# Performance work log

Hardware: AMD Instinct MI355X
Metric: run time of the kernel (lower is better)

The kernel has to match this reference:

```python
import jax, jax.numpy as jnp
import numpy as np

CONF_THRES = 0.1
IOU_THRES = 0.6
MAX_DET = 300
MAX_WH = 4096.0  # class offset for non-agnostic NMS
NEG_SLOPE = 0.01  # nn.LeakyReLU default


def xywh2xyxy(p):
    xy, wh = p[..., :2], p[..., 2:4]
    return jnp.concatenate([xy - wh / 2, xy + wh / 2], axis=-1)


def pairwise_iou(a, b):
    area_a = (a[:, 2] - a[:, 0]) * (a[:, 3] - a[:, 1])
    area_b = (b[:, 2] - b[:, 0]) * (b[:, 3] - b[:, 1])
    lt = jnp.maximum(a[:, None, :2], b[None, :, :2])
    rb = jnp.minimum(a[:, None, 2:], b[None, :, 2:])
    wh = jnp.clip(rb - lt, 0.0)
    inter = wh[..., 0] * wh[..., 1]
    return inter / (area_a[:, None] + area_b[None, :] - inter + 1e-7)


def nms_single(pred):  # pred: [N, 5+nc]
    boxes = xywh2xyxy(pred[:, :4])
    scores = pred[:, 5:] * pred[:, 4:5]  # obj * cls
    conf = jnp.max(scores, axis=1)
    cls = jnp.argmax(scores, axis=1)
    conf = jnp.where(conf > CONF_THRES, conf, 0.0)
    topv, topi = jax.lax.top_k(conf, MAX_DET)
    b = boxes[topi]                      # [K,4]
    c = cls[topi]
    valid = topv > CONF_THRES
    bo = b + (c.astype(b.dtype) * MAX_WH)[:, None]  # class-offset boxes
    iou = pairwise_iou(bo, bo)           # [K,K]
    idx = jnp.arange(MAX_DET)
    def body(i, keep):
        sup = keep[i] & (iou[i] > IOU_THRES) & (idx > i)
        return keep & ~sup
    keep = jax.lax.fori_loop(0, MAX_DET, body, valid)
    return b, keep


def bilinear_sample(feat, y, x):  # feat [C,H,W], y/x [K,P] -> [C,K,P]
    C, H, W = feat.shape
    y = jnp.clip(y, 0.0, H - 1.0)
    x = jnp.clip(x, 0.0, W - 1.0)
    y0 = jnp.floor(y).astype(jnp.int32)
    x0 = jnp.floor(x).astype(jnp.int32)
    y1 = jnp.minimum(y0 + 1, H - 1)
    x1 = jnp.minimum(x0 + 1, W - 1)
    ly = y - y0
    lx = x - x0
    return (feat[:, y0, x0] * ((1 - ly) * (1 - lx))
            + feat[:, y0, x1] * ((1 - ly) * lx)
            + feat[:, y1, x0] * (ly * (1 - lx))
            + feat[:, y1, x1] * (ly * lx))


def roi_align_1x1(feat, boxes, scale):  # feat [C,H,W], boxes [K,4] xyxy (input-px)
    b = boxes * scale
    w = jnp.maximum(b[:, 2] - b[:, 0], 1.0)
    h = jnp.maximum(b[:, 3] - b[:, 1], 1.0)
    off = jnp.array([0.5, 1.5], dtype=boxes.dtype)
    xs = b[:, 0:1] + off[None, :] * (w[:, None] / 2.0)  # [K,2]
    ys = b[:, 1:2] + off[None, :] * (h[:, None] / 2.0)
    yy = ys[:, jnp.array([0, 0, 1, 1])]  # [K,4] 2x2 grid
    xx = xs[:, jnp.array([0, 1, 0, 1])]
    v = bilinear_sample(feat, yy, xx)    # [C,K,4]
    return jnp.mean(v, axis=2).T         # [K,C]


def rescale_boxes(bbox, hw, hw0):  # scale_coords + normalize by orig shape
    gain = jnp.minimum(hw[0] / hw0[0], hw[1] / hw0[1])
    pad_x = (hw[1] - hw0[1] * gain) / 2.0
    pad_y = (hw[0] - hw0[0] * gain) / 2.0
    x1 = jnp.clip((bbox[:, 0] - pad_x) / gain, 0.0, hw0[1])
    y1 = jnp.clip((bbox[:, 1] - pad_y) / gain, 0.0, hw0[0])
    x2 = jnp.clip((bbox[:, 2] - pad_x) / gain, 0.0, hw0[1])
    y2 = jnp.clip((bbox[:, 3] - pad_y) / gain, 0.0, hw0[0])
    # divide by shapes[i][0] indexed [w,h,w,h]
    return jnp.stack([x1 / hw0[1], y1 / hw0[0], x2 / hw0[1], y2 / hw0[0]], axis=1)


def setup_inputs() -> dict:
    key = jax.random.key(0)
    ks = jax.random.split(key, 10)
    B, N, NC = 8, 25500, 80
    xy = jax.random.uniform(ks[0], (B, N, 2), minval=0.0, maxval=640.0)
    wh = jax.random.uniform(ks[1], (B, N, 2), minval=8.0, maxval=160.0)
    obj = jax.random.uniform(ks[2], (B, N, 1))
    cls = jax.random.uniform(ks[3], (B, N, NC))
    preds = jnp.concatenate([xy, wh, obj, cls], axis=-1)
    feat1 = jax.random.normal(ks[4], (B, 128, 80, 80), dtype=jnp.float32)
    feat2 = jax.random.normal(ks[5], (B, 256, 40, 40), dtype=jnp.float32)
    feat3 = jax.random.normal(ks[6], (B, 512, 20, 20), dtype=jnp.float32)
    feat4 = jax.random.normal(ks[7], (B, 1024, 10, 10), dtype=jnp.float32)
    orig_hw = jnp.tile(jnp.array([[720.0, 1280.0]], dtype=jnp.float32), (B, 1))
    W1 = jax.random.normal(ks[8], (1920, 256), dtype=jnp.float32) * 0.02
    b1 = jnp.zeros((256,), dtype=jnp.float32)
    W2 = jax.random.normal(ks[9], (256, 256), dtype=jnp.float32) * 0.02
    b2 = jnp.zeros((256,), dtype=jnp.float32)
    return {"preds": preds, "feat1": feat1, "feat2": feat2, "feat3": feat3,
            "feat4": feat4, "orig_hw": orig_hw, "W1": W1, "b1": b1,
            "W2": W2, "b2": b2}


def reference(preds, feat1, feat2, feat3, feat4, orig_hw, W1, b1, W2, b2):
    preds = jax.lax.stop_gradient(preds)  # out.detach() in the original
    hw = jnp.array(feat1.shape[-2:], dtype=preds.dtype) * 8.0  # network input h,w
    boxes, keep = jax.vmap(nms_single)(preds)  # [B,K,4], [B,K]
    f1 = jax.vmap(lambda f, b: roi_align_1x1(f, b, 1.0 / 8))(feat1, boxes)
    f2 = jax.vmap(lambda f, b: roi_align_1x1(f, b, 1.0 / 16))(feat2, boxes)
    f3 = jax.vmap(lambda f, b: roi_align_1x1(f, b, 1.0 / 32))(feat3, boxes)
    f4 = jax.vmap(lambda f, b: roi_align_1x1(f, b, 1.0 / 64))(feat4, boxes)
    f = jnp.concatenate([f1, f2, f3, f4], axis=-1)  # [B,K,1920]
    h = jax.nn.leaky_relu(f @ W1 + b1, NEG_SLOPE)
    h = jax.nn.leaky_relu(h @ W2 + b2, NEG_SLOPE)   # [B,K,256]
    bb = jax.vmap(lambda b, s: rescale_boxes(b, hw, s))(boxes, orig_hw)
    out = jnp.concatenate([bb, h], axis=-1)  # [B,K,260]
    return out * keep[..., None].astype(out.dtype)
```

## Files before the change

kernel.cpp:

```cpp
#include <hip/hip_runtime.h>
#include <hip/hip_bf16.h>
#include <cstdint>
#include <cstddef>

#define NBATCH 8
#define NANCH 25500
#define MAXDET 300
#define NBINS 2048
#define CAP 2048

typedef __bf16 bf16x8 __attribute__((ext_vector_type(8)));
typedef float floatx4 __attribute__((ext_vector_type(4)));
typedef unsigned long long ull;

__device__ __forceinline__ int conf_bin(float v) {
  unsigned bits = __float_as_uint(v);
  int bin = (int)((bits - 0x3D800000u) >> 14);
  return bin > (NBINS - 1) ? (NBINS - 1) : bin;
}

#define CONF_TILE 64
__global__ __launch_bounds__(256) void conf_kernel(const float* __restrict__ preds,
                                                   float* __restrict__ conf,
                                                   int* __restrict__ cls,
                                                   int* __restrict__ ghist, int total) {
  if (blockIdx.x < 16) {
    #pragma unroll
    for (int k = 0; k < 4; ++k)
      ghist[blockIdx.x * 1024 + k * 256 + threadIdx.x] = 0;
  }
  __shared__ float s[CONF_TILE * 85];
  int base = blockIdx.x * CONF_TILE;
  int nA = total - base; if (nA > CONF_TILE) nA = CONF_TILE;
  int n4 = (nA * 85) >> 2;
  const float4* g4 = (const float4*)(preds + (size_t)base * 85);
  float4* s4 = (float4*)s;
  for (int i = threadIdx.x; i < n4; i += 256) s4[i] = g4[i];
  __syncthreads();
  int lane16 = threadIdx.x & 15;
  int sub = threadIdx.x >> 4;
  #pragma unroll
  for (int r = 0; r < 4; ++r) {
    int a = r * 16 + sub;
    if (a < nA) {
      const float* row = s + a * 85;
      float obj = row[4];
      float best = -1.0f; int bc = 0;
      #pragma unroll
      for (int j = 0; j < 5; ++j) {
        int c = lane16 * 5 + j;
        float v = row[5 + c] * obj;
        if (v > best) { best = v; bc = c; }
      }
      #pragma unroll
      for (int m = 1; m < 16; m <<= 1) {
        float ov = __shfl_xor(best, m, 64);
        int   oc = __shfl_xor(bc,   m, 64);
        if (ov > best || (ov == best && oc < bc)) { best = ov; bc = oc; }
      }
      if (lane16 == 0) {
        int idx = base + a;
        conf[idx] = (best > 0.1f) ? best : 0.0f;
        cls[idx] = bc;
      }
    }
  }
}

struct TransArgs {
  const float* src[6];
  __hip_bfloat16* dst[6];
  int C[6], HW[6], tx[6], tpb[6], start[6];
};

__global__ void transpose_all_kernel(TransArgs a, const float* __restrict__ conf,
                                     int* __restrict__ ghist) {
  __shared__ __align__(16) char msm[8192];
  int bid = blockIdx.x;
  if (bid < 64) {
    int* sh = (int*)msm;
    int b = bid >> 3, seg = bid & 7;
    int tid = threadIdx.y * 32 + threadIdx.x;
    for (int i = tid; i < NBINS; i += 256) sh[i] = 0;
    __syncthreads();
    const int N4 = NANCH >> 2;
    int i0 = (N4 * seg) >> 3, i1 = (N4 * (seg + 1)) >> 3;
    const float4* cf4 = (const float4*)(conf + (size_t)b * NANCH);
    for (int i = i0 + tid; i < i1; i += 256) {
      float4 v = cf4[i];
      if (v.x > 0.1f) atomicAdd(&sh[conf_bin(v.x)], 1);
      if (v.y > 0.1f) atomicAdd(&sh[conf_bin(v.y)], 1);
      if (v.z > 0.1f) atomicAdd(&sh[conf_bin(v.z)], 1);
      if (v.w > 0.1f) atomicAdd(&sh[conf_bin(v.w)], 1);
    }
    __syncthreads();
    for (int i = tid; i < NBINS; i += 256) {
      int c = sh[i];
      if (c) atomicAdd(&ghist[b * NBINS + i], c);
    }
    return;
  }
  int bid2 = bid - 64;
  float (*tile)[33] = (float(*)[33])msm;
  int s = 0;
  #pragma unroll
  for (int i = 1; i < 6; ++i) if (bid2 >= a.start[i]) s = i;
  int local = bid2 - a.start[s];
  int C = a.C[s], HW = a.HW[s], tx0 = a.tx[s], tpb = a.tpb[s];
  int b = local / tpb;
  int rem = local - b * tpb;
  int p0 = (rem % tx0) * 32;
  int c0 = (rem / tx0) * 32;
  const float* inb = a.src[s] + (size_t)b * C * HW;
  __hip_bfloat16* outb = a.dst[s] + (size_t)b * C * HW;
  int tx = threadIdx.x, ty = threadIdx.y;
  #pragma unroll
  for (int k = 0; k < 32; k += 8) {
    int c = c0 + ty + k, p = p0 + tx;
    if (c < C && p < HW) tile[ty + k][tx] = inb[(size_t)c * HW + p];
  }
  __syncthreads();
  #pragma unroll
  for (int k = 0; k < 32; k += 8) {
    int p = p0 + ty + k, c = c0 + tx;
    if (p < HW && c < C) outb[(size_t)p * C + c] = __float2bfloat16(tile[tx][ty + k]);
  }
}

__global__ __launch_bounds__(1024) void nms_kernel(const float* __restrict__ conf,
                                                   const float* __restrict__ preds,
                                                   const int* __restrict__ clsg,
                                                   const int* __restrict__ ghist,
                                                   float* __restrict__ cand_v, int* __restrict__ cand_i,
                                                   float* __restrict__ boxesWs, int* __restrict__ keepWs,
                                                   const float* __restrict__ orig_hw,
                                                   float* __restrict__ out) {
  #pragma clang fp contract(off)
  __shared__ __align__(16) char smem[46592];
  int*    s_h  = (int*)smem;
  int*    s_p  = (int*)(smem + 8192);
  int*    s_ctr= (int*)(smem + 12288);
  ull   (*mask)[5] = (ull(*)[5])(smem + 8192);
  float*  lv_s = (float*)(smem + 20480);
  int*    li_s = (int*)(smem + 28672);
  float4* bo4  = (float4*)(smem + 36864);
  float (*bxx)[4] = (float(*)[4])(smem + 41664);
  ull* keepw = (ull*)(smem + 46464);
  ull* nzrow = (ull*)(smem + 46504);
  int* shv   = (int*)(smem + 46544);
  int b = blockIdx.x;
  int t = threadIdx.x;

  for (int i = t; i < NBINS; i += 1024) s_h[i] = ghist[b * NBINS + i];
  if (t < 300) {
    bo4[t] = make_float4(0.0f, 0.0f, 0.0f, 0.0f);
    bxx[t][0] = 0.0f; bxx[t][1] = 0.0f; bxx[t][2] = 0.0f; bxx[t][3] = 0.0f;
  }
  if (t == 0) shv[0] = NBINS;
  if (t < 5) nzrow[t] = 0ULL;
  __syncthreads();

  int base = t * 2;
  int v0 = s_h[base], v1 = s_h[base + 1];
  s_p[t] = v0 + v1;
  __syncthreads();
  for (int off = 1; off < 1024; off <<= 1) {
    int v = (t + off < 1024) ? s_p[t + off] : 0;
    __syncthreads();
    s_p[t] += v;
    __syncthreads();
  }
  int total = s_p[0];
  int above = (t < 1023) ? s_p[t + 1] : 0;
  s_h[base + 1] = v1 + above;
  s_h[base]     = v0 + v1 + above;
  __syncthreads();

  int nvalid = total < 300 ? total : 300;
  int target = nvalid;
  if (total > 0) {
    int sv = s_h[base], nx = s_h[base + 1];
    int nx2 = (base + 2 < NBINS) ? s_h[base + 2] : 0;
    if (sv >= target && nx  < target) shv[0] = base;
    if (nx >= target && nx2 < target) shv[0] = base + 1;
  }
  s_ctr[base]     = s_h[base + 1];
  s_ctr[base + 1] = (base + 2 < NBINS) ? s_h[base + 2] : 0;
  if (t >= nvalid && t < 300) {
    size_t bi = ((size_t)(b * 300 + t)) * 4;
    boxesWs[bi + 0] = 0.0f; boxesWs[bi + 1] = 0.0f;
    boxesWs[bi + 2] = 0.0f; boxesWs[bi + 3] = 0.0f;
  }
  if (t < 5) {
    int n = nvalid - t * 64;
    keepw[t] = (n <= 0) ? 0ULL : (n >= 64 ? ~0ULL : ((1ULL << n) - 1ULL));
  }
  __syncthreads();
  int T = shv[0];
  int Kslots = (T < NBINS) ? s_h[T] : 0;

  {
    const float4* cf4 = (const float4*)(conf + (size_t)b * NANCH);
    const int N4 = NANCH >> 2;
    float* cv = cand_v + (size_t)b * NANCH;
    int*   ci = cand_i + (size_t)b * NANCH;
    if (total > 0) {
      for (int i4 = t; i4 < N4; i4 += 1024) {
        float4 v4 = cf4[i4];
        int i0 = i4 * 4;
        float vv[4] = {v4.x, v4.y, v4.z, v4.w};
        #pragma unroll
        for (int q = 0; q < 4; ++q) {
          float v = vv[q];
          if (v > 0.1f) {
            int bin = conf_bin(v);
            if (bin >= T) {
              int slot = atomicAdd(&s_ctr[bin], 1);
              if (slot < CAP) { lv_s[slot] = v; li_s[slot] = i0 + q; }
              else            { cv[slot] = v;   ci[slot] = i0 + q;   }
            }
          }
        }
      }
    }
  }
  __syncthreads();

  {
    const float* cv = cand_v + (size_t)b * NANCH;
    const int*   ci = cand_i + (size_t)b * NANCH;
    for (int sIdx = t; sIdx < Kslots; sIdx += 1024) {
      float v; int id;
      if (sIdx < CAP) { v = lv_s[sIdx]; id = li_s[sIdx]; }
      else            { v = cv[sIdx];   id = ci[sIdx];   }
      int bin = conf_bin(v);
      int lo = (bin + 1 < NBINS) ? s_h[bin + 1] : 0;
      int hi = s_h[bin];
      int rank = lo;
      for (int j = lo; j < hi; ++j) {
        float vj; int ij;
        if (j < CAP) { vj = lv_s[j]; ij = li_s[j]; }
        else         { vj = cv[j];   ij = ci[j];   }
        rank += (int)((vj > v) | ((vj == v) & (ij < id)));
      }
      if (rank < 300) {
        const float* p = preds + ((size_t)b * NANCH + id) * 85;
        float cx = p[0], cy = p[1], w = p[2], h = p[3];
        float hw2 = w * 0.5f, hh2 = h * 0.5f;
        float x1 = cx - hw2, y1 = cy - hh2, x2 = cx + hw2, y2 = cy + hh2;
        bxx[rank][0] = x1; bxx[rank][1] = y1; bxx[rank][2] = x2; bxx[rank][3] = y2;
        size_t bi = ((size_t)(b * 300 + rank)) * 4;
        boxesWs[bi + 0] = x1; boxesWs[bi + 1] = y1;
        boxesWs[bi + 2] = x2; boxesWs[bi + 3] = y2;
        int c = clsg[(size_t)b * NANCH + id];
        float off = (float)c * 4096.0f;
        float4 ob; ob.x = x1 + off; ob.y = y1 + off; ob.z = x2 + off; ob.w = y2 + off;
        bo4[rank] = ob;
      }
    }
  }
  __syncthreads();

  {
    int wv = t >> 6, ln = t & 63;
    if (wv < 10) {
      int w = wv >> 1, half = wv & 1;
      int j = w * 64 + ln;
      int jc = j < 300 ? j : 0;
      float4 jb = bo4[jc];
      float ja = (jb.z - jb.x) * (jb.w - jb.y);
      bool jv = j < 300;
      int iend = w * 64 + 64; if (iend > 300) iend = 300;
      int i0 = half * 150, i1 = i0 + 150; if (i1 > iend) i1 = iend;
      #pragma unroll 4
      for (int i = i0; i < i1; ++i) {
        float4 ib = bo4[i];
        float ai = (ib.z - ib.x) * (ib.w - ib.y);
        float ltx = fmaxf(ib.x, jb.x);
        float lty = fmaxf(ib.y, jb.y);
        float rbx = fminf(ib.z, jb.z);
        float rby = fminf(ib.w, jb.w);
        float wx = fmaxf(rbx - ltx, 0.0f);
        float wy = fmaxf(rby - lty, 0.0f);
        float inter = wx * wy;
        float iou = inter / (ai + ja - inter + 1e-7f);
        ull bal = __ballot(jv && (j > i) && (iou > 0.6f));
        if (ln == 0) {
          mask[i][w] = bal;
          if (bal) atomicOr(&nzrow[i >> 6], 1ULL << (i & 63));
        }
      }
    }
  }
  __syncthreads();
  if (t == 0) {
    ull kw[5], nz[5];
    #pragma unroll
    for (int w = 0; w < 5; ++w) { kw[w] = keepw[w]; nz[w] = nzrow[w]; }
    #pragma unroll
    for (int w = 0; w < 5; ++w) {
      ull p = kw[w] & nz[w];
      while (p) {
        int l = __builtin_ctzll(p);
        p &= p - 1;
        int i = w * 64 + l;
        for (int w2 = w; w2 < 5; ++w2) {
          ull m = mask[i][w2];
          kw[w2] &= ~m;
          if (w2 == w) p &= ~m;
        }
      }
    }
    #pragma unroll
    for (int w = 0; w < 5; ++w) keepw[w] = kw[w];
  }
  __syncthreads();
  if (t < 300) {
    int kp = (int)((keepw[t >> 6] >> (t & 63)) & 1ULL);
    keepWs[b * 300 + t] = kp;
    float oh = orig_hw[b * 2 + 0], ow = orig_hw[b * 2 + 1];
    float gain = fminf(640.0f / oh, 640.0f / ow);
    float padx = (640.0f - ow * gain) * 0.5f;
    float pady = (640.0f - oh * gain) * 0.5f;
    float x1 = fminf(fmaxf((bxx[t][0] - padx) / gain, 0.0f), ow) / ow;
    float y1 = fminf(fmaxf((bxx[t][1] - pady) / gain, 0.0f), oh) / oh;
    float x2 = fminf(fmaxf((bxx[t][2] - padx) / gain, 0.0f), ow) / ow;
    float y2 = fminf(fmaxf((bxx[t][3] - pady) / gain, 0.0f), oh) / oh;
    size_t o = ((size_t)(b * 300 + t)) * 260;
    out[o + 0] = kp ? x1 : 0.0f;
    out[o + 1] = kp ? y1 : 0.0f;
    out[o + 2] = kp ? x2 : 0.0f;
    out[o + 3] = kp ? y2 : 0.0f;
  }
}

__global__ __launch_bounds__(256) void roi_kernel(const float* __restrict__ boxes,
                                                  const __hip_bfloat16* __restrict__ fT1, const __hip_bfloat16* __restrict__ fT2,
                                                  const __hip_bfloat16* __restrict__ fT3, const __hip_bfloat16* __restrict__ fT4,
                                                  __hip_bfloat16* __restrict__ f) {
  int b = blockIdx.x & 7;
  int r = blockIdx.x >> 3;
  __shared__ int t_off[4][16];
  __shared__ float t_w[4][16];
  int t = threadIdx.x;
  const int Hs[4] = {80, 40, 20, 10};
  const int Cs[4] = {128, 256, 512, 1024};
  const float ss[4] = {0.125f, 0.0625f, 0.03125f, 0.015625f};
  size_t bbase = ((size_t)(b * 300 + r)) * 4;
  float bx0 = boxes[bbase + 0];
  float by0 = boxes[bbase + 1];
  float bx1 = boxes[bbase + 2];
  float by1 = boxes[bbase + 3];
  if (t < 64) {
    int lv = t >> 4, k = t & 15, pp = k >> 2, nb = k & 3;
    float s = ss[lv];
    int H = Hs[lv], W = Hs[lv], C = Cs[lv];
    float b0 = bx0 * s, b1 = by0 * s, b2 = bx1 * s, b3 = by1 * s;
    float w = fmaxf(b2 - b0, 1.0f), h = fmaxf(b3 - b1, 1.0f);
    const float offv[2] = {0.5f, 1.5f};
    float px = b0 + offv[pp & 1] * (w * 0.5f);
    float py = b1 + offv[pp >> 1] * (h * 0.5f);
    float y = fminf(fmaxf(py, 0.0f), (float)(H - 1));
    float x = fminf(fmaxf(px, 0.0f), (float)(W - 1));
    int y0 = (int)floorf(y), x0 = (int)floorf(x);
    int y1 = min(y0 + 1, H - 1), x1 = min(x0 + 1, W - 1);
    float ly = y - (float)y0, lx = x - (float)x0;
    int yy = (nb & 2) ? y1 : y0;
    int xx = (nb & 1) ? x1 : x0;
    float wy = (nb & 2) ? ly : (1.0f - ly);
    float wx = (nb & 1) ? lx : (1.0f - lx);
    t_off[lv][k] = (yy * W + xx) * C;
    t_w[lv][k] = wy * wx;
  }
  __syncthreads();
  const __hip_bfloat16* bases[4] = {
    fT1 + (size_t)b * 6400 * 128,
    fT2 + (size_t)b * 1600 * 256,
    fT3 + (size_t)b * 400 * 512,
    fT4 + (size_t)b * 100 * 1024
  };
  __hip_bfloat16* frow = f + (size_t)(b * 300 + r) * 1920;
  int cbase = 0;
  #pragma unroll
  for (int lv = 0; lv < 4; ++lv) {
    int C = Cs[lv];
    const __hip_bfloat16* base = bases[lv];
    for (int c = t; c < C; c += 256) {
      float acc = 0.0f;
      #pragma unroll
      for (int k = 0; k < 16; ++k)
        acc += t_w[lv][k] * __bfloat162float(base[t_off[lv][k] + c]);
      frow[cbase + c] = __float2bfloat16(acc * 0.25f);
    }
    cbase += C;
  }
}

#define GLDS16(gp, lp) __builtin_amdgcn_global_load_lds( \
    (const __attribute__((address_space(1))) unsigned int*)(gp), \
    (__attribute__((address_space(3))) unsigned int*)(lp), 16, 0, 0)

__global__ __launch_bounds__(256) void gemm_tile_kernel(const __hip_bfloat16* __restrict__ A,
                                                        const __hip_bfloat16* __restrict__ BT,
                                                        const float* __restrict__ bias,
                                                        __hip_bfloat16* __restrict__ Cb,
                                                        float* __restrict__ Cf,
                                                        const int* __restrict__ keep,
                                                        int M, int N, int K, int ldc, int coff) {
  __shared__ __hip_bfloat16 sA[2][64 * 64];
  __shared__ __hip_bfloat16 sB[2][64 * 64];
  int tid = threadIdx.x;
  int bm = blockIdx.x * 64, bn = blockIdx.y * 64;
  int wave = tid >> 6, lane = tid & 63;
  int wr = wave >> 1, wc = wave & 1;
  int idx16 = lane & 15, kb = lane >> 4;
  floatx4 acc[2][2] = {};
  int nt = K >> 6;

  auto stage = [&](int buf, int t) {
    int k0 = t << 6;
    #pragma unroll
    for (int i = 0; i < 2; ++i) {
      int c = tid + i * 256;
      int row = c >> 3, cc = c & 7;
      int scc = cc ^ (row & 7);
      GLDS16(A + (size_t)(bm + row) * K + k0 + scc * 8,
             (char*)&sA[buf][0] + c * 16);
    }
    #pragma unroll
    for (int i = 0; i < 2; ++i) {
      int c = tid + i * 256;
      int row = c >> 3, cc = c & 7;
      int scc = cc ^ (row & 7);
      GLDS16(BT + (size_t)(bn + row) * K + k0 + scc * 8,
             (char*)&sB[buf][0] + c * 16);
    }
  };

  stage(0, 0);
  asm volatile("s_waitcnt vmcnt(0)" ::: "memory");
  __syncthreads();
  int cur = 0;
  for (int t = 0; t < nt; ++t) {
    if (t + 1 < nt) stage(cur ^ 1, t + 1);
    const char* Ab = (const char*)&sA[cur][0];
    const char* Bb = (const char*)&sB[cur][0];
    #pragma unroll
    for (int s = 0; s < 2; ++s) {
      bf16x8 af[2], bg[2];
      #pragma unroll
      for (int m = 0; m < 2; ++m) {
        int row = wr * 32 + m * 16 + idx16;
        int chunk = s * 4 + kb;
        af[m] = *(const bf16x8*)(Ab + row * 128 + ((chunk ^ (row & 7)) * 16));
      }
      #pragma unroll
      for (int n = 0; n < 2; ++n) {
        int row = wc * 32 + n * 16 + idx16;
        int chunk = s * 4 + kb;
        bg[n] = *(const bf16x8*)(Bb + row * 128 + ((chunk ^ (row & 7)) * 16));
      }
      #pragma unroll
      for (int m = 0; m < 2; ++m)
        #pragma unroll
        for (int n = 0; n < 2; ++n)
          acc[m][n] = __builtin_amdgcn_mfma_f32_16x16x32_bf16(af[m], bg[n], acc[m][n], 0, 0, 0);
    }
    asm volatile("s_waitcnt vmcnt(0)" ::: "memory");
    __syncthreads();
    cur ^= 1;
  }
  int col = lane & 15, rb4 = (lane >> 4) * 4;
  #pragma unroll
  for (int m = 0; m < 2; ++m) {
    #pragma unroll
    for (int n = 0; n < 2; ++n) {
      #pragma unroll
      for (int r = 0; r < 4; ++r) {
        int orow = bm + wr * 32 + m * 16 + rb4 + r;
        int ocol = bn + wc * 32 + n * 16 + col;
        if (orow >= M) continue;
        float v = acc[m][n][r] + bias[ocol];
        v = (v >= 0.0f) ? v : 0.01f * v;
        if (Cb) Cb[(size_t)orow * N + ocol] = __float2bfloat16(v);
        if (Cf) {
          float km = keep ? (keep[orow] ? 1.0f : 0.0f) : 1.0f;
          Cf[(size_t)orow * ldc + coff + ocol] = v * km;
        }
      }
    }
  }
}

extern "C" void kernel_launch(void* const* d_in, const int* in_sizes, int n_in,
                              void* d_out, int out_size, void* d_ws, size_t ws_size,
                              hipStream_t stream) {
  (void)in_sizes; (void)n_in; (void)out_size; (void)ws_size;
  const float* preds  = (const float*)d_in[0];
  const float* feat1  = (const float*)d_in[1];
  const float* feat2  = (const float*)d_in[2];
  const float* feat3  = (const float*)d_in[3];
  const float* feat4  = (const float*)d_in[4];
  const float* orighw = (const float*)d_in[5];
  const float* W1     = (const float*)d_in[6];
  const float* b1     = (const float*)d_in[7];
  const float* W2     = (const float*)d_in[8];
  const float* b2     = (const float*)d_in[9];
  float* out = (float*)d_out;

  char* ws = (char*)d_ws;
  size_t off = 0;
  auto alloc = [&](size_t bytes) -> void* {
    void* p = ws + off;
    off = (off + bytes + 255) & ~(size_t)255;
    return p;
  };
  const int BN = NBATCH * NANCH;
  float*  conf   = (float*)alloc((size_t)BN * 4);
  int*    cls    = (int*)  alloc((size_t)BN * 4);
  float*  cand_v = (float*)alloc((size_t)BN * 4);
  int*    cand_i = (int*)  alloc((size_t)BN * 4);
  int*    ghist  = (int*)  alloc((size_t)NBATCH * NBINS * 4);
  float*  boxes  = (float*)alloc((size_t)NBATCH * 300 * 4 * 4);
  int*    keep   = (int*)  alloc((size_t)NBATCH * 300 * 4);
  __hip_bfloat16* fT1  = (__hip_bfloat16*)alloc((size_t)NBATCH * 6400 * 128 * 2);
  __hip_bfloat16* fT2  = (__hip_bfloat16*)alloc((size_t)NBATCH * 1600 * 256 * 2);
  __hip_bfloat16* fT3  = (__hip_bfloat16*)alloc((size_t)NBATCH * 400 * 512 * 2);
  __hip_bfloat16* fT4  = (__hip_bfloat16*)alloc((size_t)NBATCH * 100 * 1024 * 2);
  __hip_bfloat16* fmat = (__hip_bfloat16*)alloc((size_t)2400 * 1920 * 2);
  __hip_bfloat16* h1b  = (__hip_bfloat16*)alloc((size_t)2400 * 256 * 2);
  __hip_bfloat16* W1T  = (__hip_bfloat16*)alloc((size_t)256 * 1920 * 2);
  __hip_bfloat16* W2T  = (__hip_bfloat16*)alloc((size_t)256 * 256 * 2);

  conf_kernel<<<(BN + CONF_TILE - 1) / CONF_TILE, 256, 0, stream>>>(preds, conf, cls, ghist, BN);

  TransArgs ta;
  ta.src[0] = feat1; ta.dst[0] = fT1; ta.C[0] = 128;  ta.HW[0] = 6400; ta.tx[0] = 200;
  ta.src[1] = feat2; ta.dst[1] = fT2; ta.C[1] = 256;  ta.HW[1] = 1600; ta.tx[1] = 50;
  ta.src[2] = feat3; ta.dst[2] = fT3; ta.C[2] = 512;  ta.HW[2] = 400;  ta.tx[2] = 13;
  ta.src[3] = feat4; ta.dst[3] = fT4; ta.C[3] = 1024; ta.HW[3] = 100;  ta.tx[3] = 4;
  ta.src[4] = W1;    ta.dst[4] = W1T; ta.C[4] = 1920; ta.HW[4] = 256;  ta.tx[4] = 8;
  ta.src[5] = W2;    ta.dst[5] = W2T; ta.C[5] = 256;  ta.HW[5] = 256;  ta.tx[5] = 8;
  int total_blocks = 0;
  for (int s = 0; s < 6; ++s) {
    int ty = (ta.C[s] + 31) / 32;
    int nbatch = (s < 4) ? NBATCH : 1;
    ta.tpb[s] = ta.tx[s] * ty;
    ta.start[s] = total_blocks;
    total_blocks += ta.tpb[s] * nbatch;
  }
  transpose_all_kernel<<<total_blocks + 64, dim3(32, 8), 0, stream>>>(ta, conf, ghist);

  nms_kernel<<<NBATCH, 1024, 0, stream>>>(conf, preds, cls, ghist, cand_v, cand_i,
                                          boxes, keep, orighw, out);
  roi_kernel<<<2400, 256, 0, stream>>>(boxes, fT1, fT2, fT3, fT4, fmat);
  gemm_tile_kernel<<<dim3(38, 4), 256, 0, stream>>>(fmat, W1T, b1, h1b, nullptr, nullptr,
                                                    2400, 256, 1920, 0, 0);
  gemm_tile_kernel<<<dim3(38, 4), 256, 0, stream>>>(h1b, W2T, b2, nullptr, out, keep,
                                                    2400, 256, 256, 260, 4);
}
```

Before: 133.3 us.

## Fuse NMS into transpose/histogram kernel with a global-counter spin-wait

Merges the histogram, feature/weight transpose and NMS stages into one persistent-style launch. The first 8 blocks spin on a global counter until the 64 histogram blocks finish, then run NMS while the transpose blocks proceed concurrently. The block-prefix scan over bins is replaced with wave-level shuffle scans, and transpose blocks are widened to 1024 threads handling 4 tiles each. This saves a launch and overlaps the serial NMS with the bandwidth-bound transpose. In exchange it relies on the histogram blocks being scheduled alongside the spinning blocks, which is a forward-progress risk.

```diff
diff --git a/kernel.cpp b/kernel.cpp
--- a/kernel.cpp
+++ b/kernel.cpp
@@ -23,12 +23,14 @@
 __global__ __launch_bounds__(256) void conf_kernel(const float* __restrict__ preds,
                                                    float* __restrict__ conf,
                                                    int* __restrict__ cls,
-                                                   int* __restrict__ ghist, int total) {
+                                                   int* __restrict__ ghist,
+                                                   int* __restrict__ ctr, int total) {
   if (blockIdx.x < 16) {
     #pragma unroll
     for (int k = 0; k < 4; ++k)
       ghist[blockIdx.x * 1024 + k * 256 + threadIdx.x] = 0;
   }
+  if (blockIdx.x == 16 && threadIdx.x == 0) ctr[0] = 0;
   __shared__ float s[CONF_TILE * 85];
   int base = blockIdx.x * CONF_TILE;
   int nA = total - base; if (nA > CONF_TILE) nA = CONF_TILE;
@@ -73,20 +75,249 @@
   int C[6], HW[6], tx[6], tpb[6], start[6];
 };
 
-__global__ void transpose_all_kernel(TransArgs a, const float* __restrict__ conf,
-                                     int* __restrict__ ghist) {
-  __shared__ __align__(16) char msm[8192];
+__global__ __launch_bounds__(1024) void mid_kernel(TransArgs a,
+                                                   const float* __restrict__ conf,
+                                                   const float* __restrict__ preds,
+                                                   const int* __restrict__ clsg,
+                                                   int* __restrict__ ghist,
+                                                   int* __restrict__ ctr,
+                                                   float* __restrict__ cand_v, int* __restrict__ cand_i,
+                                                   float* __restrict__ boxesWs, int* __restrict__ keepWs,
+                                                   const float* __restrict__ orig_hw,
+                                                   float* __restrict__ out,
+                                                   int n_trans_tiles) {
+  #pragma clang fp contract(off)
+  __shared__ __align__(16) char smem[42496];
   int bid = blockIdx.x;
-  if (bid < 64) {
-    int* sh = (int*)msm;
-    int b = bid >> 3, seg = bid & 7;
-    int tid = threadIdx.y * 32 + threadIdx.x;
-    for (int i = tid; i < NBINS; i += 256) sh[i] = 0;
+  int t = threadIdx.y * 32 + threadIdx.x;
+
+  if (bid < 8) {
+    int b = bid;
+    int*    s_h  = (int*)smem;
+    int*    s_ctr= (int*)(smem + 8192);
+    ull   (*mask)[5] = (ull(*)[5])smem;
+    float*  lv_s = (float*)(smem + 16384);
+    int*    li_s = (int*)(smem + 24576);
+    float4* bo4  = (float4*)(smem + 32768);
+    float (*bxx)[4] = (float(*)[4])(smem + 37568);
+    ull* keepw = (ull*)(smem + 42368);
+    ull* nzrow = (ull*)(smem + 42408);
+    int* shv   = (int*)(smem + 42448);
+
+    if (t < 300) {
+      bo4[t] = make_float4(0.0f, 0.0f, 0.0f, 0.0f);
+      bxx[t][0] = 0.0f; bxx[t][1] = 0.0f; bxx[t][2] = 0.0f; bxx[t][3] = 0.0f;
+    }
+    if (t < 5) nzrow[t] = 0ULL;
+    if (t == 1) { shv[0] = NBINS; shv[2] = 0; }
+    if (t == 0) {
+      while (atomicAdd(ctr, 0) < 64) __builtin_amdgcn_s_sleep(8);
+      __threadfence();
+    }
+    __syncthreads();
+
+    int r[8], suf[8], rs[8];
+    int w = t >> 6, lane = t & 63;
+    if (t < 256) {
+      #pragma unroll
+      for (int k = 0; k < 8; ++k)
+        r[k] = atomicAdd(&ghist[b * NBINS + (w * 8 + k) * 64 + lane], 0);
+      int bsum = 0;
+      #pragma unroll
+      for (int k = 0; k < 8; ++k) {
+        int s = r[k];
+        #pragma unroll
+        for (int d = 1; d < 64; d <<= 1) {
+          int o = __shfl_down(s, d, 64);
+          if (lane + d < 64) s += o;
+        }
+        suf[k] = s - r[k];
+        rs[k] = __shfl(s, 0, 64);
+        bsum += rs[k];
+      }
+      if (lane == 0) shv[4 + w] = bsum;
+    }
+    __syncthreads();
+    if (t < 256) {
+      int p1 = shv[5], p2 = shv[6], p3 = shv[7];
+      int total = shv[4] + p1 + p2 + p3;
+      int target = total < 300 ? total : 300;
+      int RS = (w == 0) ? (p1 + p2 + p3) : (w == 1) ? (p2 + p3) : (w == 2) ? p3 : 0;
+      int run = RS;
+      #pragma unroll
+      for (int k = 7; k >= 0; --k) {
+        int Sx = run + suf[k] + r[k];
+        int Sx1 = Sx - r[k];
+        int bin = (w * 8 + k) * 64 + lane;
+        s_h[bin] = Sx;
+        s_ctr[bin] = Sx1;
+        if (total > 0 && Sx >= target && Sx1 < target) { shv[0] = bin; shv[2] = Sx; }
+        run += rs[k];
+      }
+      if (t == 0) shv[1] = total;
+    }
+    __syncthreads();
+    int T = shv[0];
+    int total = shv[1];
+    int Kslots = shv[2];
+    int nvalid = total < 300 ? total : 300;
+
+    if (t >= nvalid && t < 300) {
+      size_t bi = ((size_t)(b * 300 + t)) * 4;
+      boxesWs[bi + 0] = 0.0f; boxesWs[bi + 1] = 0.0f;
+      boxesWs[bi + 2] = 0.0f; boxesWs[bi + 3] = 0.0f;
+    }
+    if (t < 5) {
+      int n = nvalid - t * 64;
+      keepw[t] = (n <= 0) ? 0ULL : (n >= 64 ? ~0ULL : ((1ULL << n) - 1ULL));
+    }
+
+    {
+      const float4* cf4 = (const float4*)(conf + (size_t)b * NANCH);
+      const int N4 = NANCH >> 2;
+      float* cv = cand_v + (size_t)b * NANCH;
+      int*   ci = cand_i + (size_t)b * NANCH;
+      if (total > 0) {
+        for (int i4 = t; i4 < N4; i4 += 1024) {
+          float4 v4 = cf4[i4];
+          int i0 = i4 * 4;
+          float vv[4] = {v4.x, v4.y, v4.z, v4.w};
+          #pragma unroll
+          for (int q = 0; q < 4; ++q) {
+            float v = vv[q];
+            if (v > 0.1f) {
+              int bin = conf_bin(v);
+              if (bin >= T) {
+                int slot = atomicAdd(&s_ctr[bin], 1);
+                if (slot < CAP) { lv_s[slot] = v; li_s[slot] = i0 + q; }
+                else            { cv[slot] = v;   ci[slot] = i0 + q;   }
+              }
+            }
+          }
+        }
+      }
+    }
+    __syncthreads();
+
+    {
+      const float* cv = cand_v + (size_t)b * NANCH;
+      const int*   ci = cand_i + (size_t)b * NANCH;
+      for (int sIdx = t; sIdx < Kslots; sIdx += 1024) {
+        float v; int id;
+        if (sIdx < CAP) { v = lv_s[sIdx]; id = li_s[sIdx]; }
+        else            { v = cv[sIdx];   id = ci[sIdx];   }
+        int bin = conf_bin(v);
+        int lo = (bin + 1 < NBINS) ? s_h[bin + 1] : 0;
+        int hi = s_h[bin];
+        int rank = lo;
+        for (int j = lo; j < hi; ++j) {
+          float vj; int ij;
+          if (j < CAP) { vj = lv_s[j]; ij = li_s[j]; }
+          else         { vj = cv[j];   ij = ci[j];   }
+          rank += (int)((vj > v) | ((vj == v) & (ij < id)));
+        }
+        if (rank < 300) {
+          const float* p = preds + ((size_t)b * NANCH + id) * 85;
+          float cx = p[0], cy = p[1], wq = p[2], hq = p[3];
+          float hw2 = wq * 0.5f, hh2 = hq * 0.5f;
+          float x1 = cx - hw2, y1 = cy - hh2, x2 = cx + hw2, y2 = cy + hh2;
+          bxx[rank][0] = x1; bxx[rank][1] = y1; bxx[rank][2] = x2; bxx[rank][3] = y2;
+          size_t bi = ((size_t)(b * 300 + rank)) * 4;
+          boxesWs[bi + 0] = x1; boxesWs[bi + 1] = y1;
+          boxesWs[bi + 2] = x2; boxesWs[bi + 3] = y2;
+          int c = clsg[(size_t)b * NANCH + id];
+          float off = (float)c * 4096.0f;
+          float4 ob; ob.x = x1 + off; ob.y = y1 + off; ob.z = x2 + off; ob.w = y2 + off;
+          bo4[rank] = ob;
+        }
+      }
+    }
+    __syncthreads();
+
+    {
+      int wv = t >> 6, ln = t & 63;
+      if (wv < 10) {
+        int w2 = wv >> 1, half = wv & 1;
+        int j = w2 * 64 + ln;
+        int jc = j < 300 ? j : 0;
+        float4 jb = bo4[jc];
+        float ja = (jb.z - jb.x) * (jb.w - jb.y);
+        bool jv = j < 300;
+        int iend = w2 * 64 + 64; if (iend > 300) iend = 300;
+        int i0 = half * 150, i1 = i0 + 150; if (i1 > iend) i1 = iend;
+        #pragma unroll 4
+        for (int i = i0; i < i1; ++i) {
+          float4 ib = bo4[i];
+          float ai = (ib.z - ib.x) * (ib.w - ib.y);
+          float ltx = fmaxf(ib.x, jb.x);
+          float lty = fmaxf(ib.y, jb.y);
+          float rbx = fminf(ib.z, jb.z);
+          float rby = fminf(ib.w, jb.w);
+          float wx = fmaxf(rbx - ltx, 0.0f);
+          float wy = fmaxf(rby - lty, 0.0f);
+          float inter = wx * wy;
+          float iou = inter / (ai + ja - inter + 1e-7f);
+          ull bal = __ballot(jv && (j > i) && (iou > 0.6f));
+          if (ln == 0) {
+            mask[i][w2] = bal;
+            if (bal) atomicOr(&nzrow[i >> 6], 1ULL << (i & 63));
+          }
+        }
+      }
+    }
+    __syncthreads();
+    if (t == 0) {
+      ull kw[5], nz[5];
+      #pragma unroll
+      for (int w2 = 0; w2 < 5; ++w2) { kw[w2] = keepw[w2]; nz[w2] = nzrow[w2]; }
+      #pragma unroll
+      for (int w2 = 0; w2 < 5; ++w2) {
+        ull p = kw[w2] & nz[w2];
+        while (p) {
+          int l = __builtin_ctzll(p);
+          p &= p - 1;
+          int i = w2 * 64 + l;
+          for (int w3 = w2; w3 < 5; ++w3) {
+            ull m = mask[i][w3];
+            kw[w3] &= ~m;
+            if (w3 == w2) p &= ~m;
+          }
+        }
+      }
+      #pragma unroll
+      for (int w2 = 0; w2 < 5; ++w2) keepw[w2] = kw[w2];
+    }
+    __syncthreads();
+    if (t < 300) {
+      int kp = (int)((keepw[t >> 6] >> (t & 63)) & 1ULL);
+      keepWs[b * 300 + t] = kp;
+      float oh = orig_hw[b * 2 + 0], ow = orig_hw[b * 2 + 1];
+      float gain = fminf(640.0f / oh, 640.0f / ow);
+      float padx = (640.0f - ow * gain) * 0.5f;
+      float pady = (640.0f - oh * gain) * 0.5f;
+      float x1 = fminf(fmaxf((bxx[t][0] - padx) / gain, 0.0f), ow) / ow;
+      float y1 = fminf(fmaxf((bxx[t][1] - pady) / gain, 0.0f), oh) / oh;
+      float x2 = fminf(fmaxf((bxx[t][2] - padx) / gain, 0.0f), ow) / ow;
+      float y2 = fminf(fmaxf((bxx[t][3] - pady) / gain, 0.0f), oh) / oh;
+      size_t o = ((size_t)(b * 300 + t)) * 260;
+      out[o + 0] = kp ? x1 : 0.0f;
+      out[o + 1] = kp ? y1 : 0.0f;
+      out[o + 2] = kp ? x2 : 0.0f;
+      out[o + 3] = kp ? y2 : 0.0f;
+    }
+    return;
+  }
+
+  if (bid < 72) {
+    int hb = bid - 8;
+    int b = hb >> 3, seg = hb & 7;
+    int* sh = (int*)smem;
+    sh[t] = 0; sh[t + 1024] = 0;
     __syncthreads();
     const int N4 = NANCH >> 2;
     int i0 = (N4 * seg) >> 3, i1 = (N4 * (seg + 1)) >> 3;
     const float4* cf4 = (const float4*)(conf + (size_t)b * NANCH);
-    for (int i = i0 + tid; i < i1; i += 256) {
+    for (int i = i0 + t; i < i1; i += 1024) {
       float4 v = cf4[i];
       if (v.x > 0.1f) atomicAdd(&sh[conf_bin(v.x)], 1);
       if (v.y > 0.1f) atomicAdd(&sh[conf_bin(v.y)], 1);
@@ -94,243 +325,50 @@
       if (v.w > 0.1f) atomicAdd(&sh[conf_bin(v.w)], 1);
     }
     __syncthreads();
-    for (int i = tid; i < NBINS; i += 256) {
-      int c = sh[i];
-      if (c) atomicAdd(&ghist[b * NBINS + i], c);
-    }
+    {
+      int c = sh[t];        if (c) atomicAdd(&ghist[b * NBINS + t], c);
+      c     = sh[t + 1024]; if (c) atomicAdd(&ghist[b * NBINS + t + 1024], c);
+    }
+    __syncthreads();
+    if (t == 0) { __threadfence(); atomicAdd(ctr, 1); }
     return;
   }
-  int bid2 = bid - 64;
-  float (*tile)[33] = (float(*)[33])msm;
-  int s = 0;
-  #pragma unroll
-  for (int i = 1; i < 6; ++i) if (bid2 >= a.start[i]) s = i;
-  int local = bid2 - a.start[s];
-  int C = a.C[s], HW = a.HW[s], tx0 = a.tx[s], tpb = a.tpb[s];
-  int b = local / tpb;
-  int rem = local - b * tpb;
-  int p0 = (rem % tx0) * 32;
-  int c0 = (rem / tx0) * 32;
-  const float* inb = a.src[s] + (size_t)b * C * HW;
-  __hip_bfloat16* outb = a.dst[s] + (size_t)b * C * HW;
-  int tx = threadIdx.x, ty = threadIdx.y;
-  #pragma unroll
-  for (int k = 0; k < 32; k += 8) {
-    int c = c0 + ty + k, p = p0 + tx;
-    if (c < C && p < HW) tile[ty + k][tx] = inb[(size_t)c * HW + p];
-  }
-  __syncthreads();
-  #pragma unroll
-  for (int k = 0; k < 32; k += 8) {
-    int p = p0 + ty + k, c = c0 + tx;
-    if (p < HW && c < C) outb[(size_t)p * C + c] = __float2bfloat16(tile[tx][ty + k]);
-  }
-}
-
-__global__ __launch_bounds__(1024) void nms_kernel(const float* __restrict__ conf,
-                                                   const float* __restrict__ preds,
-                                                   const int* __restrict__ clsg,
-                                                   const int* __restrict__ ghist,
-                                                   float* __restrict__ cand_v, int* __restrict__ cand_i,
-                                                   float* __restrict__ boxesWs, int* __restrict__ keepWs,
-                                                   const float* __restrict__ orig_hw,
-                                                   float* __restrict__ out) {
-  #pragma clang fp contract(off)
-  __shared__ __align__(16) char smem[46592];
-  int*    s_h  = (int*)smem;
-  int*    s_p  = (int*)(smem + 8192);
-  int*    s_ctr= (int*)(smem + 12288);
-  ull   (*mask)[5] = (ull(*)[5])(smem + 8192);
-  float*  lv_s = (float*)(smem + 20480);
-  int*    li_s = (int*)(smem + 28672);
-  float4* bo4  = (float4*)(smem + 36864);
-  float (*bxx)[4] = (float(*)[4])(smem + 41664);
-  ull* keepw = (ull*)(smem + 46464);
-  ull* nzrow = (ull*)(smem + 46504);
-  int* shv   = (int*)(smem + 46544);
-  int b = blockIdx.x;
-  int t = threadIdx.x;
-
-  for (int i = t; i < NBINS; i += 1024) s_h[i] = ghist[b * NBINS + i];
-  if (t < 300) {
-    bo4[t] = make_float4(0.0f, 0.0f, 0.0f, 0.0f);
-    bxx[t][0] = 0.0f; bxx[t][1] = 0.0f; bxx[t][2] = 0.0f; bxx[t][3] = 0.0f;
-  }
-  if (t == 0) shv[0] = NBINS;
-  if (t < 5) nzrow[t] = 0ULL;
-  __syncthreads();
-
-  int base = t * 2;
-  int v0 = s_h[base], v1 = s_h[base + 1];
-  s_p[t] = v0 + v1;
-  __syncthreads();
-  for (int off = 1; off < 1024; off <<= 1) {
-    int v = (t + off < 1024) ? s_p[t + off] : 0;
-    __syncthreads();
-    s_p[t] += v;
-    __syncthreads();
-  }
-  int total = s_p[0];
-  int above = (t < 1023) ? s_p[t + 1] : 0;
-  s_h[base + 1] = v1 + above;
-  s_h[base]     = v0 + v1 + above;
-  __syncthreads();
-
-  int nvalid = total < 300 ? total : 300;
-  int target = nvalid;
-  if (total > 0) {
-    int sv = s_h[base], nx = s_h[base + 1];
-    int nx2 = (base + 2 < NBINS) ? s_h[base + 2] : 0;
-    if (sv >= target && nx  < target) shv[0] = base;
-    if (nx >= target && nx2 < target) shv[0] = base + 1;
-  }
-  s_ctr[base]     = s_h[base + 1];
-  s_ctr[base + 1] = (base + 2 < NBINS) ? s_h[base + 2] : 0;
-  if (t >= nvalid && t < 300) {
-    size_t bi = ((size_t)(b * 300 + t)) * 4;
-    boxesWs[bi + 0] = 0.0f; boxesWs[bi + 1] = 0.0f;
-    boxesWs[bi + 2] = 0.0f; boxesWs[bi + 3] = 0.0f;
-  }
-  if (t < 5) {
-    int n = nvalid - t * 64;
-    keepw[t] = (n <= 0) ? 0ULL : (n >= 64 ? ~0ULL : ((1ULL << n) - 1ULL));
-  }
-  __syncthreads();
-  int T = shv[0];
-  int Kslots = (T < NBINS) ? s_h[T] : 0;
 
   {
-    const float4* cf4 = (const float4*)(conf + (size_t)b * NANCH);
-    const int N4 = NANCH >> 2;
-    float* cv = cand_v + (size_t)b * NANCH;
-    int*   ci = cand_i + (size_t)b * NANCH;
-    if (total > 0) {
-      for (int i4 = t; i4 < N4; i4 += 1024) {
-        float4 v4 = cf4[i4];
-        int i0 = i4 * 4;
-        float vv[4] = {v4.x, v4.y, v4.z, v4.w};
-        #pragma unroll
-        for (int q = 0; q < 4; ++q) {
-          float v = vv[q];
-          if (v > 0.1f) {
-            int bin = conf_bin(v);
-            if (bin >= T) {
-              int slot = atomicAdd(&s_ctr[bin], 1);
-              if (slot < CAP) { lv_s[slot] = v; li_s[slot] = i0 + q; }
-              else            { cv[slot] = v;   ci[slot] = i0 + q;   }
-            }
-          }
-        }
-      }
-    }
-  }
-  __syncthreads();
-
-  {
-    const float* cv = cand_v + (size_t)b * NANCH;
-    const int*   ci = cand_i + (size_t)b * NANCH;
-    for (int sIdx = t; sIdx < Kslots; sIdx += 1024) {
-      float v; int id;
-      if (sIdx < CAP) { v = lv_s[sIdx]; id = li_s[sIdx]; }
-      else            { v = cv[sIdx];   id = ci[sIdx];   }
-      int bin = conf_bin(v);
-      int lo = (bin + 1 < NBINS) ? s_h[bin + 1] : 0;
-      int hi = s_h[bin];
-      int rank = lo;
-      for (int j = lo; j < hi; ++j) {
-        float vj; int ij;
-        if (j < CAP) { vj = lv_s[j]; ij = li_s[j]; }
-        else         { vj = cv[j];   ij = ci[j];   }
-        rank += (int)((vj > v) | ((vj == v) & (ij < id)));
-      }
-      if (rank < 300) {
-        const float* p = preds + ((size_t)b * NANCH + id) * 85;
-        float cx = p[0], cy = p[1], w = p[2], h = p[3];
-        float hw2 = w * 0.5f, hh2 = h * 0.5f;
-        float x1 = cx - hw2, y1 = cy - hh2, x2 = cx + hw2, y2 = cy + hh2;
-        bxx[rank][0] = x1; bxx[rank][1] = y1; bxx[rank][2] = x2; bxx[rank][3] = y2;
-        size_t bi = ((size_t)(b * 300 + rank)) * 4;
-        boxesWs[bi + 0] = x1; boxesWs[bi + 1] = y1;
-        boxesWs[bi + 2] = x2; boxesWs[bi + 3] = y2;
-        int c = clsg[(size_t)b * NANCH + id];
-        float off = (float)c * 4096.0f;
-        float4 ob; ob.x = x1 + off; ob.y = y1 + off; ob.z = x2 + off; ob.w = y2 + off;
-        bo4[rank] = ob;
-      }
-    }
-  }
-  __syncthreads();
-
-  {
-    int wv = t >> 6, ln = t & 63;
-    if (wv < 10) {
-      int w = wv >> 1, half = wv & 1;
-      int j = w * 64 + ln;
-      int jc = j < 300 ? j : 0;
-      float4 jb = bo4[jc];
-      float ja = (jb.z - jb.x) * (jb.w - jb.y);
-      bool jv = j < 300;
-      int iend = w * 64 + 64; if (iend > 300) iend = 300;
-      int i0 = half * 150, i1 = i0 + 150; if (i1 > iend) i1 = iend;
-      #pragma unroll 4
-      for (int i = i0; i < i1; ++i) {
-        float4 ib = bo4[i];
-        float ai = (ib.z - ib.x) * (ib.w - ib.y);
-        float ltx = fmaxf(ib.x, jb.x);
-        float lty = fmaxf(ib.y, jb.y);
-        float rbx = fminf(ib.z, jb.z);
-        float rby = fminf(ib.w, jb.w);
-        float wx = fmaxf(rbx - ltx, 0.0f);
-        float wy = fmaxf(rby - lty, 0.0f);
-        float inter = wx * wy;
-        float iou = inter / (ai + ja - inter + 1e-7f);
-        ull bal = __ballot(jv && (j > i) && (iou > 0.6f));
-        if (ln == 0) {
-          mask[i][w] = bal;
-          if (bal) atomicOr(&nzrow[i >> 6], 1ULL << (i & 63));
-        }
-      }
-    }
-  }
-  __syncthreads();
-  if (t == 0) {
-    ull kw[5], nz[5];
-    #pragma unroll
-    for (int w = 0; w < 5; ++w) { kw[w] = keepw[w]; nz[w] = nzrow[w]; }
-    #pragma unroll
-    for (int w = 0; w < 5; ++w) {
-      ull p = kw[w] & nz[w];
-      while (p) {
-        int l = __builtin_ctzll(p);
-        p &= p - 1;
-        int i = w * 64 + l;
-        for (int w2 = w; w2 < 5; ++w2) {
-          ull m = mask[i][w2];
-          kw[w2] &= ~m;
-          if (w2 == w) p &= ~m;
-        }
-      }
-    }
-    #pragma unroll
-    for (int w = 0; w < 5; ++w) keepw[w] = kw[w];
-  }
-  __syncthreads();
-  if (t < 300) {
-    int kp = (int)((keepw[t >> 6] >> (t & 63)) & 1ULL);
-    keepWs[b * 300 + t] = kp;
-    float oh = orig_hw[b * 2 + 0], ow = orig_hw[b * 2 + 1];
-    float gain = fminf(640.0f / oh, 640.0f / ow);
-    float padx = (640.0f - ow * gain) * 0.5f;
-    float pady = (640.0f - oh * gain) * 0.5f;
-    float x1 = fminf(fmaxf((bxx[t][0] - padx) / gain, 0.0f), ow) / ow;
-    float y1 = fminf(fmaxf((bxx[t][1] - pady) / gain, 0.0f), oh) / oh;
-    float x2 = fminf(fmaxf((bxx[t][2] - padx) / gain, 0.0f), ow) / ow;
-    float y2 = fminf(fmaxf((bxx[t][3] - pady) / gain, 0.0f), oh) / oh;
-    size_t o = ((size_t)(b * 300 + t)) * 260;
-    out[o + 0] = kp ? x1 : 0.0f;
-    out[o + 1] = kp ? y1 : 0.0f;
-    out[o + 2] = kp ? x2 : 0.0f;
-    out[o + 3] = kp ? y2 : 0.0f;
+    int sub = threadIdx.y >> 3;
+    int tyl = threadIdx.y & 7, tx = threadIdx.x;
+    int gt = (bid - 72) * 4 + sub;
+    float (*tile)[33] = (float(*)[33])(smem + sub * 4224);
+    int s = 0, local = 0, C = 0, HW = 0, p0 = 0, c0 = 0, bb = 0;
+    const float* inb = nullptr;
+    __hip_bfloat16* outb = nullptr;
+    bool act = gt < n_trans_tiles;
+    if (act) {
+      #pragma unroll
+      for (int i = 1; i < 6; ++i) if (gt >= a.start[i]) s = i;
+      local = gt - a.start[s];
+      C = a.C[s]; HW = a.HW[s];
+      int tx0 = a.tx[s], tpb = a.tpb[s];
+      bb = local / tpb;
+      int rem = local - bb * tpb;
+      p0 = (rem % tx0) * 32;
+      c0 = (rem / tx0) * 32;
+      inb = a.src[s] + (size_t)bb * C * HW;
+      outb = a.dst[s] + (size_t)bb * C * HW;
+      #pragma unroll
+      for (int k = 0; k < 32; k += 8) {
+        int c = c0 + tyl + k, p = p0 + tx;
+        if (c < C && p < HW) tile[tyl + k][tx] = inb[(size_t)c * HW + p];
+      }
+    }
+    __syncthreads();
+    if (act) {
+      #pragma unroll
+      for (int k = 0; k < 32; k += 8) {
+        int p = p0 + tyl + k, c = c0 + tx;
+        if (p < HW && c < C) outb[(size_t)p * C + c] = __float2bfloat16(tile[tx][tyl + k]);
+      }
+    }
   }
 }
 
@@ -521,6 +559,7 @@
   float*  cand_v = (float*)alloc((size_t)BN * 4);
   int*    cand_i = (int*)  alloc((size_t)BN * 4);
   int*    ghist  = (int*)  alloc((size_t)NBATCH * NBINS * 4);
+  int*    ctr    = (int*)  alloc(256);
   float*  boxes  = (float*)alloc((size_t)NBATCH * 300 * 4 * 4);
   int*    keep   = (int*)  alloc((size_t)NBATCH * 300 * 4);
   __hip_bfloat16* fT1  = (__hip_bfloat16*)alloc((size_t)NBATCH * 6400 * 128 * 2);
@@ -532,7 +571,7 @@
   __hip_bfloat16* W1T  = (__hip_bfloat16*)alloc((size_t)256 * 1920 * 2);
   __hip_bfloat16* W2T  = (__hip_bfloat16*)alloc((size_t)256 * 256 * 2);
 
-  conf_kernel<<<(BN + CONF_TILE - 1) / CONF_TILE, 256, 0, stream>>>(preds, conf, cls, ghist, BN);
+  conf_kernel<<<(BN + CONF_TILE - 1) / CONF_TILE, 256, 0, stream>>>(preds, conf, cls, ghist, ctr, BN);
 
   TransArgs ta;
   ta.src[0] = feat1; ta.dst[0] = fT1; ta.C[0] = 128;  ta.HW[0] = 6400; ta.tx[0] = 200;
@@ -541,18 +580,19 @@
   ta.src[3] = feat4; ta.dst[3] = fT4; ta.C[3] = 1024; ta.HW[3] = 100;  ta.tx[3] = 4;
   ta.src[4] = W1;    ta.dst[4] = W1T; ta.C[4] = 1920; ta.HW[4] = 256;  ta.tx[4] = 8;
   ta.src[5] = W2;    ta.dst[5] = W2T; ta.C[5] = 256;  ta.HW[5] = 256;  ta.tx[5] = 8;
-  int total_blocks = 0;
+  int n_tiles = 0;
   for (int s = 0; s < 6; ++s) {
     int ty = (ta.C[s] + 31) / 32;
     int nbatch = (s < 4) ? NBATCH : 1;
     ta.tpb[s] = ta.tx[s] * ty;
-    ta.start[s] = total_blocks;
-    total_blocks += ta.tpb[s] * nbatch;
-  }
-  transpose_all_kernel<<<total_blocks + 64, dim3(32, 8), 0, stream>>>(ta, conf, ghist);
-
-  nms_kernel<<<NBATCH, 1024, 0, stream>>>(conf, preds, cls, ghist, cand_v, cand_i,
-                                          boxes, keep, orighw, out);
+    ta.start[s] = n_tiles;
+    n_tiles += ta.tpb[s] * nbatch;
+  }
+  int mid_grid = 72 + (n_tiles + 3) / 4;
+  mid_kernel<<<mid_grid, dim3(32, 32), 0, stream>>>(ta, conf, preds, cls, ghist, ctr,
+                                                    cand_v, cand_i, boxes, keep, orighw, out,
+                                                    n_tiles);
+
   roi_kernel<<<2400, 256, 0, stream>>>(boxes, fT1, fT2, fT3, fT4, fmat);
   gemm_tile_kernel<<<dim3(38, 4), 256, 0, stream>>>(fmat, W1T, b1, h1b, nullptr, nullptr,
                                                     2400, 256, 1920, 0, 0);
```

Measured after the change: 118.5 us. -11.1%, faster.
